# Kernel tuning notes

Hardware: AMD Instinct MI355X
Metric: run time of the kernel (lower is better)

Reference implementation:

```python
import jax, jax.numpy as jnp
import numpy as np
from jax import lax


def _qconv_w(r, i, j, k):
    # Hamilton-product block kernel: components are (out/4, in/4, kh, kw) -> (out, in, kh, kw)
    row_r = jnp.concatenate([r, -i, -j, -k], axis=1)
    row_i = jnp.concatenate([i, r, -k, j], axis=1)
    row_j = jnp.concatenate([j, k, r, -i], axis=1)
    row_k = jnp.concatenate([k, -j, i, r], axis=1)
    return jnp.concatenate([row_r, row_i, row_j, row_k], axis=0)


def _conv3x3(x, W, b):
    y = lax.conv_general_dilated(x, W, window_strides=(1, 1), padding=((1, 1), (1, 1)),
                                 dimension_numbers=('NCHW', 'OIHW', 'NCHW'))
    return y + b[None, :, None, None]


def _qbn(x, gamma, beta, eps=1e-5):
    # Quaternion BN: global per-component mean, shared scalar quaternion variance
    r, i, j, k = jnp.split(x, 4, axis=1)
    dr, di, dj, dk = r - r.mean(), i - i.mean(), j - j.mean(), k - k.mean()
    var = (dr * dr + di * di + dj * dj + dk * dk).mean()
    inv = 1.0 / jnp.sqrt(var + eps)
    br, bi, bj, bk = jnp.split(beta, 4, axis=1)
    return jnp.concatenate([gamma * dr * inv + br, gamma * di * inv + bi,
                            gamma * dj * inv + bj, gamma * dk * inv + bk], axis=1)


def _pool2(x):
    b, c, h, w = x.shape
    return x.reshape(b, c, h // 2, 2, w // 2, 2).mean(axis=(3, 5))


def _qlin_w(r, i, j, k):
    # components (in/4, out/4) -> (in, out)
    col_r = jnp.concatenate([r, -i, -j, -k], axis=0)
    col_i = jnp.concatenate([i, r, -k, j], axis=0)
    col_j = jnp.concatenate([j, k, r, -i], axis=0)
    col_k = jnp.concatenate([k, -j, i, r], axis=0)
    return jnp.concatenate([col_r, col_i, col_j, col_k], axis=1)


def _forward(x, w_eca, l1_r, l1_i, l1_j, l1_k, l1_b, bn1_gamma, bn1_beta,
             l2_r, l2_i, l2_j, l2_k, l2_b, bn2_gamma, bn2_beta,
             l3_r, l3_i, l3_j, l3_k, l3_b, bn3_gamma, bn3_beta,
             fc_r, fc_i, fc_j, fc_k, fc_b):
    # ---- pre_press: eca_layer(k_size=1) top-3 channel selection + zero quaternion channel
    pooled = x.mean(axis=(2, 3))                      # [B, C] global avg pool
    att = jax.nn.softmax(w_eca[0] * pooled, axis=1)   # 1x1 conv1d == scalar scale, softmax over channels
    _, idx = lax.top_k(att, 3)                        # sorted descending, matches torch.topk
    top3 = jnp.take_along_axis(x, idx[:, :, None, None], axis=1)  # [B, 3, H, W]
    q = jnp.concatenate([jnp.zeros_like(top3[:, :1]), top3], axis=1)  # [B, 4, H, W]
    # ---- QConvEtAl: only layer1..3 are used in forward
    h = _conv3x3(q, _qconv_w(l1_r, l1_i, l1_j, l1_k), l1_b)
    h = _pool2(jax.nn.relu(_qbn(h, bn1_gamma, bn1_beta)))
    h = _conv3x3(h, _qconv_w(l2_r, l2_i, l2_j, l2_k), l2_b)
    h = _pool2(jax.nn.relu(_qbn(h, bn2_gamma, bn2_beta)))
    h = _conv3x3(h, _qconv_w(l3_r, l3_i, l3_j, l3_k), l3_b)
    h = _pool2(jax.nn.relu(_qbn(h, bn3_gamma, bn3_beta)))
    h = h.reshape(h.shape[0], -1)                     # [B, 128*(P/8)^2]
    return h @ _qlin_w(fc_r, fc_i, fc_j, fc_k) + fc_b


def setup_inputs() -> dict:
    key = jax.random.key(0)
    ks = jax.random.split(key, 20)
    rn = lambda k, s, sc=0.1: (jax.random.normal(k, s) * sc).astype(jnp.float32)
    inp = {
        'x': jax.random.normal(ks[0], (256, 200, 32, 32), dtype=jnp.float32),
        'w_eca': rn(ks[1], (1,), 1.0),
        'l1_r': rn(ks[2], (4, 1, 3, 3)), 'l1_i': rn(ks[3], (4, 1, 3, 3)),
        'l1_j': rn(ks[4], (4, 1, 3, 3)), 'l1_k': rn(ks[5], (4, 1, 3, 3)),
        'l1_b': jnp.zeros((16,), jnp.float32),
        'bn1_gamma': jnp.ones((1, 4, 1, 1), jnp.float32), 'bn1_beta': jnp.zeros((1, 16, 1, 1), jnp.float32),
        'l2_r': rn(ks[6], (16, 4, 3, 3)), 'l2_i': rn(ks[7], (16, 4, 3, 3)),
        'l2_j': rn(ks[8], (16, 4, 3, 3)), 'l2_k': rn(ks[9], (16, 4, 3, 3)),
        'l2_b': jnp.zeros((64,), jnp.float32),
        'bn2_gamma': jnp.ones((1, 16, 1, 1), jnp.float32), 'bn2_beta': jnp.zeros((1, 64, 1, 1), jnp.float32),
        'l3_r': rn(ks[10], (32, 16, 3, 3)), 'l3_i': rn(ks[11], (32, 16, 3, 3)),
        'l3_j': rn(ks[12], (32, 16, 3, 3)), 'l3_k': rn(ks[13], (32, 16, 3, 3)),
        'l3_b': jnp.zeros((128,), jnp.float32),
        'bn3_gamma': jnp.ones((1, 32, 1, 1), jnp.float32), 'bn3_beta': jnp.zeros((1, 128, 1, 1), jnp.float32),
        'fc_r': rn(ks[14], (512, 4)), 'fc_i': rn(ks[15], (512, 4)),
        'fc_j': rn(ks[16], (512, 4)), 'fc_k': rn(ks[17], (512, 4)),
        'fc_b': jnp.zeros((16,), jnp.float32),
    }
    return inp


def reference(x, w_eca, l1_r, l1_i, l1_j, l1_k, l1_b, bn1_gamma, bn1_beta,
              l2_r, l2_i, l2_j, l2_k, l2_b, bn2_gamma, bn2_beta,
              l3_r, l3_i, l3_j, l3_k, l3_b, bn3_gamma, bn3_beta,
              fc_r, fc_i, fc_j, fc_k, fc_b):
    return _forward(x, w_eca, l1_r, l1_i, l1_j, l1_k, l1_b, bn1_gamma, bn1_beta,
                    l2_r, l2_i, l2_j, l2_k, l2_b, bn2_gamma, bn2_beta,
                    l3_r, l3_i, l3_j, l3_k, l3_b, bn3_gamma, bn3_beta,
                    fc_r, fc_i, fc_j, fc_k, fc_b)
```

## Files before the change

### kernel.cpp

```cpp
#include <hip/hip_runtime.h>
#include <math.h>

#define WS_STATS 0
#define WS_W1    32
#define WS_W2    640
#define WS_W3    9856
#define WS_WFC   83584
#define WS_POOL  116352
#define WS_IDX   167552
#define WS_OUT1  168448
#define WS_P1    4362752
#define WS_OUT3  5411328
#define WS_P3    7508480

__device__ const int   d_TC[4][4] = {{0,1,2,3},{1,0,3,2},{2,3,0,1},{3,2,1,0}};
__device__ const float d_TS[4][4] = {{1.f,-1.f,-1.f,-1.f},{1.f,1.f,-1.f,1.f},
                                     {1.f,1.f,1.f,-1.f},{1.f,-1.f,1.f,1.f}};

__global__ __launch_bounds__(256) void prep_kernel(
    const float* l1r, const float* l1i, const float* l1j, const float* l1k,
    const float* l2r, const float* l2i, const float* l2j, const float* l2k,
    const float* l3r, const float* l3i, const float* l3j, const float* l3k,
    const float* fcr, const float* fci, const float* fcj, const float* fck,
    float* ws)
{
    int tid  = blockIdx.x * 256 + threadIdx.x;
    int nthr = gridDim.x * 256;
    if (tid < 24) ws[WS_STATS + tid] = 0.f;

    {
        const float* cp[4] = {l1r, l1i, l1j, l1k};
        for (int e = tid; e < 576; e += nthr) {
            int s = e / 144, rem = e % 144, k = rem / 16, oc = rem % 16;
            int p = oc >> 2, o = oc & 3;
            ws[WS_W1 + e] = d_TS[p][s] * cp[d_TC[p][s]][o * 9 + k];
        }
    }
    {
        const float* cp[4] = {l2r, l2i, l2j, l2k};
        for (int e = tid; e < 9216; e += nthr) {
            int oc = e & 63, k = (e >> 6) % 9, ic = e / 576;
            int p = oc >> 4, o = oc & 15, s = ic >> 2, ii = ic & 3;
            ws[WS_W2 + e] = d_TS[p][s] * cp[d_TC[p][s]][(o * 4 + ii) * 9 + k];
        }
    }
    {
        const float* cp[4] = {l3r, l3i, l3j, l3k};
        for (int e = tid; e < 73728; e += nthr) {
            int oc = e & 127, k = (e >> 7) % 9, ic = e / 1152;
            int p = oc >> 5, o = oc & 31, s = ic >> 4, ii = ic & 15;
            ws[WS_W3 + e] = d_TS[p][s] * cp[d_TC[p][s]][(o * 16 + ii) * 9 + k];
        }
    }
    {
        const float* cp[4] = {fcr, fci, fcj, fck};
        for (int e = tid; e < 32768; e += nthr) {
            int R = e >> 4, C = e & 15;
            int p = R >> 9, rr = R & 511, q = C >> 2, cc = C & 3;
            ws[WS_WFC + e] = d_TS[q][p] * cp[d_TC[q][p]][rr * 4 + cc];
        }
    }
}

__global__ __launch_bounds__(256) void mean_kernel(const float* __restrict__ x,
                                                   float* __restrict__ pooled)
{
    int bc = blockIdx.x;
    int t  = threadIdx.x;
    const float4* src = reinterpret_cast<const float4*>(x + (size_t)bc * 1024);
    float4 v = src[t];
    float s = v.x + v.y + v.z + v.w;
    #pragma unroll
    for (int off = 32; off; off >>= 1) s += __shfl_xor(s, off, 64);
    __shared__ float red[4];
    if ((t & 63) == 0) red[t >> 6] = s;
    __syncthreads();
    if (t == 0) pooled[bc] = (red[0] + red[1] + red[2] + red[3]) * (1.0f / 1024.0f);
}

__global__ __launch_bounds__(64) void topk_kernel(const float* __restrict__ pooled,
                                                  const float* __restrict__ w_eca,
                                                  int* __restrict__ idx3)
{
    int b = blockIdx.x, lane = threadIdx.x;
    float w = w_eca[0];
    float v[4]; int c[4];
    #pragma unroll
    for (int i = 0; i < 4; i++) {
        int ch = lane + 64 * i;
        c[i] = ch;
        v[i] = (ch < 200) ? w * pooled[b * 200 + ch] : -INFINITY;
    }
    for (int k = 0; k < 3; k++) {
        float bv = -INFINITY; int bi = 0x3fffffff;
        #pragma unroll
        for (int i = 0; i < 4; i++)
            if (v[i] > bv || (v[i] == bv && c[i] < bi)) { bv = v[i]; bi = c[i]; }
        for (int off = 32; off; off >>= 1) {
            float ov = __shfl_xor(bv, off, 64);
            int   oi = __shfl_xor(bi, off, 64);
            if (ov > bv || (ov == bv && oi < bi)) { bv = ov; bi = oi; }
        }
        if (lane == 0) idx3[b * 3 + k] = bi;
        #pragma unroll
        for (int i = 0; i < 4; i++) if (c[i] == bi) v[i] = -INFINITY;
    }
}

__global__ __launch_bounds__(256) void conv1_kernel(const float* __restrict__ x,
                                                    const int* __restrict__ idx3,
                                                    const float* __restrict__ W1,
                                                    const float* __restrict__ b1,
                                                    float* __restrict__ out1,
                                                    float* __restrict__ stats)
{
    __shared__ float smem[3][6][36];
    __shared__ float rs[8];
    int b = blockIdx.x >> 3, rg = blockIdx.x & 7;
    int t = threadIdx.x;
    if (t < 8) rs[t] = 0.f;
    for (int i = t; i < 648; i += 256) {
        int s = i / 216, rem = i % 216, r = rem / 36, c = rem % 36;
        int gr = rg * 4 - 1 + r, gc = c - 1;
        float v = 0.f;
        if (gr >= 0 && gr < 32 && gc >= 0 && gc < 32)
            v = x[((size_t)b * 200 + idx3[b * 3 + s]) * 1024 + gr * 32 + gc];
        smem[s][r][c] = v;
    }
    __syncthreads();

    int oc = t & 15, rp = (t >> 4) & 3, ch = t >> 6;
    float bb = b1[oc];
    float acc[8];
    #pragma unroll
    for (int px = 0; px < 8; px++) acc[px] = bb;

    #pragma unroll
    for (int s = 0; s < 3; s++) {
        float w[9];
        #pragma unroll
        for (int k = 0; k < 9; k++) w[k] = W1[((s + 1) * 9 + k) * 16 + oc];
        float rowv[3][12];
        #pragma unroll
        for (int dy = 0; dy < 3; dy++) {
            const float* rb = &smem[s][rp + dy][ch * 8];
            float4 a = *reinterpret_cast<const float4*>(rb);
            float4 bq = *reinterpret_cast<const float4*>(rb + 4);
            float4 cq = *reinterpret_cast<const float4*>(rb + 8);
            rowv[dy][0]=a.x;  rowv[dy][1]=a.y;  rowv[dy][2]=a.z;  rowv[dy][3]=a.w;
            rowv[dy][4]=bq.x; rowv[dy][5]=bq.y; rowv[dy][6]=bq.z; rowv[dy][7]=bq.w;
            rowv[dy][8]=cq.x; rowv[dy][9]=cq.y; rowv[dy][10]=cq.z; rowv[dy][11]=cq.w;
        }
        #pragma unroll
        for (int dy = 0; dy < 3; dy++)
            #pragma unroll
            for (int px = 0; px < 8; px++) {
                float a = acc[px];
                a = fmaf(w[dy*3+0], rowv[dy][px],   a);
                a = fmaf(w[dy*3+1], rowv[dy][px+1], a);
                a = fmaf(w[dy*3+2], rowv[dy][px+2], a);
                acc[px] = a;
            }
    }
    int row = rg * 4 + rp;
    float* outb = out1 + ((size_t)b * 16 + oc) * 1024 + row * 32 + ch * 8;
    *reinterpret_cast<float4*>(outb)     = make_float4(acc[0], acc[1], acc[2], acc[3]);
    *reinterpret_cast<float4*>(outb + 4) = make_float4(acc[4], acc[5], acc[6], acc[7]);
    float sv = 0.f, qv = 0.f;
    #pragma unroll
    for (int px = 0; px < 8; px++) { sv += acc[px]; qv += acc[px] * acc[px]; }
    int g = oc >> 2;
    atomicAdd(&rs[g], sv); atomicAdd(&rs[4 + g], qv);
    __syncthreads();
    if (t < 8) atomicAdd(&stats[t], rs[t]);
}

template<int C, int H, int Cq>
__global__ __launch_bounds__(256) void bnpool_kernel(const float* __restrict__ in,
                                                     float* __restrict__ out,
                                                     const float* __restrict__ stats,
                                                     const float* __restrict__ gamma,
                                                     const float* __restrict__ beta,
                                                     float invN)
{
    constexpr int Ho = H / 2;
    int o = blockIdx.x * 256 + threadIdx.x;
    float mean[4]; float var = 0.f;
    #pragma unroll
    for (int g = 0; g < 4; g++) {
        float S = stats[g], Q = stats[4 + g];
        mean[g] = S * invN;
        var += Q - S * S * invN;
    }
    var *= invN;
    float inv = 1.0f / sqrtf(var + 1e-5f);

    int xq = o % Ho;
    int yq = (o / Ho) % Ho;
    int c  = (o / (Ho * Ho)) % C;
    int b  = o / (Ho * Ho * C);
    const float* base = in + ((size_t)((b * C + c) * H + 2 * yq)) * H + 2 * xq;
    float2 v01 = *reinterpret_cast<const float2*>(base);
    float2 v23 = *reinterpret_cast<const float2*>(base + H);
    int g = c / Cq, wv = c % Cq;
    float scale = gamma[wv] * inv;
    float sh = beta[c] - mean[g] * scale;
    float r0 = fmaxf(fmaf(v01.x, scale, sh), 0.f);
    float r1 = fmaxf(fmaf(v01.y, scale, sh), 0.f);
    float r2 = fmaxf(fmaf(v23.x, scale, sh), 0.f);
    float r3 = fmaxf(fmaf(v23.y, scale, sh), 0.f);
    out[o] = 0.25f * (r0 + r1 + r2 + r3);
}

__global__ __launch_bounds__(256) void conv2_kernel(const float* __restrict__ p1,
                                                    const float* __restrict__ W2,
                                                    const float* __restrict__ b2,
                                                    float* __restrict__ out2,
                                                    float* __restrict__ stats)
{
    __shared__ float smem[16][4][20];
    __shared__ float rs[8];
    int b = blockIdx.x >> 3, rq = blockIdx.x & 7;
    int t = threadIdx.x;
    if (t < 8) rs[t] = 0.f;
    for (int i = t; i < 1280; i += 256) {
        int ic = i / 80, rem = i % 80, r = rem / 20, c = rem % 20;
        int gr = rq * 2 - 1 + r, gc = c - 1;
        float v = 0.f;
        if (gr >= 0 && gr < 16 && gc >= 0 && gc < 16)
            v = p1[((size_t)b * 16 + ic) * 256 + gr * 16 + gc];
        smem[ic][r][c] = v;
    }
    __syncthreads();

    int oc = t & 63, rp = (t >> 6) & 1, ch = t >> 7;
    float bb = b2[oc];
    float acc[8];
    #pragma unroll
    for (int px = 0; px < 8; px++) acc[px] = bb;

    const float* Wp = W2 + oc;
    for (int ic = 0; ic < 16; ic++) {
        float w[9];
        #pragma unroll
        for (int k = 0; k < 9; k++) w[k] = Wp[ic * 576 + k * 64];
        float rowv[3][12];
        #pragma unroll
        for (int dy = 0; dy < 3; dy++) {
            const float* rb = &smem[ic][rp + dy][ch * 8];
            float4 a = *reinterpret_cast<const float4*>(rb);
            float4 bq = *reinterpret_cast<const float4*>(rb + 4);
            float4 cq = *reinterpret_cast<const float4*>(rb + 8);
            rowv[dy][0]=a.x;  rowv[dy][1]=a.y;  rowv[dy][2]=a.z;  rowv[dy][3]=a.w;
            rowv[dy][4]=bq.x; rowv[dy][5]=bq.y; rowv[dy][6]=bq.z; rowv[dy][7]=bq.w;
            rowv[dy][8]=cq.x; rowv[dy][9]=cq.y; rowv[dy][10]=cq.z; rowv[dy][11]=cq.w;
        }
        #pragma unroll
        for (int dy = 0; dy < 3; dy++)
            #pragma unroll
            for (int px = 0; px < 8; px++) {
                float a = acc[px];
                a = fmaf(w[dy*3+0], rowv[dy][px],   a);
                a = fmaf(w[dy*3+1], rowv[dy][px+1], a);
                a = fmaf(w[dy*3+2], rowv[dy][px+2], a);
                acc[px] = a;
            }
    }
    int row = rq * 2 + rp;
    float* outb = out2 + ((size_t)b * 64 + oc) * 256 + row * 16 + ch * 8;
    *reinterpret_cast<float4*>(outb)     = make_float4(acc[0], acc[1], acc[2], acc[3]);
    *reinterpret_cast<float4*>(outb + 4) = make_float4(acc[4], acc[5], acc[6], acc[7]);
    float sv = 0.f, qv = 0.f;
    #pragma unroll
    for (int px = 0; px < 8; px++) { sv += acc[px]; qv += acc[px] * acc[px]; }
    int g = oc >> 4;
    atomicAdd(&rs[g], sv); atomicAdd(&rs[4 + g], qv);
    __syncthreads();
    if (t < 8) atomicAdd(&stats[t], rs[t]);
}

__global__ __launch_bounds__(256) void conv3_kernel(const float* __restrict__ p2,
                                                    const float* __restrict__ W3,
                                                    const float* __restrict__ b3,
                                                    float* __restrict__ out3,
                                                    float* __restrict__ stats)
{
    __shared__ float smem[64][4][12];
    __shared__ float rs[8];
    int b = blockIdx.x >> 2, rh = blockIdx.x & 3;
    int t = threadIdx.x;
    if (t < 8) rs[t] = 0.f;
    for (int i = t; i < 3072; i += 256) {
        int ic = i / 48, rem = i % 48, r = rem / 12, c = rem % 12;
        int gr = rh * 2 - 1 + r, gc = c - 1;
        float v = 0.f;
        if (gr >= 0 && gr < 8 && gc >= 0 && gc < 8)
            v = p2[((size_t)b * 64 + ic) * 64 + gr * 8 + gc];
        smem[ic][r][c] = v;
    }
    __syncthreads();

    int oc = t & 127, rp = t >> 7;
    float bb = b3[oc];
    float acc[8];
    #pragma unroll
    for (int px = 0; px < 8; px++) acc[px] = bb;

    const float* Wp = W3 + oc;
    float w[9], wn[9];
    #pragma unroll
    for (int k = 0; k < 9; k++) w[k] = Wp[k * 128];
    for (int ic = 0; ic < 64; ic++) {
        if (ic < 63) {
            #pragma unroll
            for (int k = 0; k < 9; k++) wn[k] = Wp[(ic + 1) * 1152 + k * 128];
        }
        float rowv[3][12];
        #pragma unroll
        for (int dy = 0; dy < 3; dy++) {
            const float* rb = &smem[ic][rp + dy][0];
            float4 a = *reinterpret_cast<const float4*>(rb);
            float4 bq = *reinterpret_cast<const float4*>(rb + 4);
            float4 cq = *reinterpret_cast<const float4*>(rb + 8);
            rowv[dy][0]=a.x;  rowv[dy][1]=a.y;  rowv[dy][2]=a.z;  rowv[dy][3]=a.w;
            rowv[dy][4]=bq.x; rowv[dy][5]=bq.y; rowv[dy][6]=bq.z; rowv[dy][7]=bq.w;
            rowv[dy][8]=cq.x; rowv[dy][9]=cq.y; rowv[dy][10]=cq.z; rowv[dy][11]=cq.w;
        }
        #pragma unroll
        for (int dy = 0; dy < 3; dy++)
            #pragma unroll
            for (int px = 0; px < 8; px++) {
                float a = acc[px];
                a = fmaf(w[dy*3+0], rowv[dy][px],   a);
                a = fmaf(w[dy*3+1], rowv[dy][px+1], a);
                a = fmaf(w[dy*3+2], rowv[dy][px+2], a);
                acc[px] = a;
            }
        if (ic < 63) {
            #pragma unroll
            for (int k = 0; k < 9; k++) w[k] = wn[k];
        }
    }
    int row = rh * 2 + rp;
    float* outb = out3 + ((size_t)b * 128 + oc) * 64 + row * 8;
    *reinterpret_cast<float4*>(outb)     = make_float4(acc[0], acc[1], acc[2], acc[3]);
    *reinterpret_cast<float4*>(outb + 4) = make_float4(acc[4], acc[5], acc[6], acc[7]);
    float sv = 0.f, qv = 0.f;
    #pragma unroll
    for (int px = 0; px < 8; px++) { sv += acc[px]; qv += acc[px] * acc[px]; }
    int g = oc >> 5;
    atomicAdd(&rs[g], sv); atomicAdd(&rs[4 + g], qv);
    __syncthreads();
    if (t < 8) atomicAdd(&stats[t], rs[t]);
}

__global__ __launch_bounds__(256) void fc_kernel(const float* __restrict__ p3,
                                                 const float* __restrict__ WFC,
                                                 const float* __restrict__ fcb,
                                                 float* __restrict__ out)
{
    int b = blockIdx.x, t = threadIdx.x;
    int col = t & 15, fr = t >> 4;
    const float* pb = p3 + (size_t)b * 2048;
    float s = 0.f;
    for (int i = 0; i < 128; i++) {
        int f = i * 16 + fr;
        s = fmaf(pb[f], WFC[f * 16 + col], s);
    }
    __shared__ float red[256];
    red[t] = s;
    __syncthreads();
    for (int st = 128; st >= 16; st >>= 1) {
        if (t < st) red[t] += red[t + st];
        __syncthreads();
    }
    if (t < 16) out[b * 16 + t] = red[t] + fcb[t];
}

extern "C" void kernel_launch(void* const* d_in, const int* in_sizes, int n_in,
                              void* d_out, int out_size, void* d_ws, size_t ws_size,
                              hipStream_t stream)
{
    (void)in_sizes; (void)n_in; (void)out_size; (void)ws_size;
    const float* x     = (const float*)d_in[0];
    const float* w_eca = (const float*)d_in[1];
    const float* l1r = (const float*)d_in[2],  *l1i = (const float*)d_in[3];
    const float* l1j = (const float*)d_in[4],  *l1k = (const float*)d_in[5];
    const float* l1b = (const float*)d_in[6];
    const float* bn1g = (const float*)d_in[7], *bn1b = (const float*)d_in[8];
    const float* l2r = (const float*)d_in[9],  *l2i = (const float*)d_in[10];
    const float* l2j = (const float*)d_in[11], *l2k = (const float*)d_in[12];
    const float* l2b = (const float*)d_in[13];
    const float* bn2g = (const float*)d_in[14], *bn2b = (const float*)d_in[15];
    const float* l3r = (const float*)d_in[16], *l3i = (const float*)d_in[17];
    const float* l3j = (const float*)d_in[18], *l3k = (const float*)d_in[19];
    const float* l3b = (const float*)d_in[20];
    const float* bn3g = (const float*)d_in[21], *bn3b = (const float*)d_in[22];
    const float* fcr = (const float*)d_in[23], *fci = (const float*)d_in[24];
    const float* fcj = (const float*)d_in[25], *fck = (const float*)d_in[26];
    const float* fcb = (const float*)d_in[27];

    float* ws   = (float*)d_ws;
    float* outp = (float*)d_out;

    prep_kernel<<<512, 256, 0, stream>>>(l1r, l1i, l1j, l1k, l2r, l2i, l2j, l2k,
                                         l3r, l3i, l3j, l3k, fcr, fci, fcj, fck, ws);
    mean_kernel<<<51200, 256, 0, stream>>>(x, ws + WS_POOL);
    topk_kernel<<<256, 64, 0, stream>>>(ws + WS_POOL, w_eca, (int*)(ws + WS_IDX));
    conv1_kernel<<<2048, 256, 0, stream>>>(x, (const int*)(ws + WS_IDX), ws + WS_W1,
                                           l1b, ws + WS_OUT1, ws + WS_STATS);
    bnpool_kernel<16, 32, 4><<<4096, 256, 0, stream>>>(ws + WS_OUT1, ws + WS_P1,
        ws + WS_STATS, bn1g, bn1b, 1.0f / 1048576.0f);
    conv2_kernel<<<2048, 256, 0, stream>>>(ws + WS_P1, ws + WS_W2, l2b,
                                           ws + WS_OUT1, ws + WS_STATS + 8);
    bnpool_kernel<64, 16, 16><<<4096, 256, 0, stream>>>(ws + WS_OUT1, ws + WS_P1,
        ws + WS_STATS + 8, bn2g, bn2b, 1.0f / 1048576.0f);
    conv3_kernel<<<1024, 256, 0, stream>>>(ws + WS_P1, ws + WS_W3, l3b,
                                           ws + WS_OUT3, ws + WS_STATS + 16);
    bnpool_kernel<128, 8, 32><<<2048, 256, 0, stream>>>(ws + WS_OUT3, ws + WS_P3,
        ws + WS_STATS + 16, bn3g, bn3b, 1.0f / 524288.0f);
    fc_kernel<<<256, 256, 0, stream>>>(ws + WS_P3, ws + WS_WFC, fcb, outp);
}
```

Baseline: 190.9 us.

## Fuse BN+pool into consumer convs, merge prep/mean and topk into conv1

Cuts the launch chain from ten kernels to five. The BN-ReLU-avgpool stages are folded into the shared-memory loads of conv2, conv3 and fc, and the weight prep is merged with the channel-mean pass. Top-k selection now runs inside each conv1 block. This removes the pooled intermediate buffers and their extra global round trips. In exchange, the top-k is recomputed redundantly in every block (8 per batch), and conv2 gets register double-buffering of its weights.

```diff
diff --git a/kernel.cpp b/kernel.cpp
--- a/kernel.cpp
+++ b/kernel.cpp
@@ -7,25 +7,38 @@
 #define WS_W3    9856
 #define WS_WFC   83584
 #define WS_POOL  116352
-#define WS_IDX   167552
-#define WS_OUT1  168448
-#define WS_P1    4362752
-#define WS_OUT3  5411328
-#define WS_P3    7508480
+#define WS_OUT1  167552
+#define WS_OUT2  4361856
+#define WS_OUT3  8556160
 
 __device__ const int   d_TC[4][4] = {{0,1,2,3},{1,0,3,2},{2,3,0,1},{3,2,1,0}};
 __device__ const float d_TS[4][4] = {{1.f,-1.f,-1.f,-1.f},{1.f,1.f,-1.f,1.f},
                                      {1.f,1.f,1.f,-1.f},{1.f,-1.f,1.f,1.f}};
 
-__global__ __launch_bounds__(256) void prep_kernel(
+__global__ __launch_bounds__(256) void prepmean_kernel(
+    const float* __restrict__ x, float* __restrict__ pooled,
     const float* l1r, const float* l1i, const float* l1j, const float* l1k,
     const float* l2r, const float* l2i, const float* l2j, const float* l2k,
     const float* l3r, const float* l3i, const float* l3j, const float* l3k,
     const float* fcr, const float* fci, const float* fcj, const float* fck,
     float* ws)
 {
-    int tid  = blockIdx.x * 256 + threadIdx.x;
-    int nthr = gridDim.x * 256;
+    __shared__ float red[4];
+    int bid = blockIdx.x;
+    int t = threadIdx.x;
+    if (bid < 51200) {
+        const float4* src = reinterpret_cast<const float4*>(x + (size_t)bid * 1024);
+        float4 v = src[t];
+        float s = v.x + v.y + v.z + v.w;
+        #pragma unroll
+        for (int off = 32; off; off >>= 1) s += __shfl_xor(s, off, 64);
+        if ((t & 63) == 0) red[t >> 6] = s;
+        __syncthreads();
+        if (t == 0) pooled[bid] = (red[0] + red[1] + red[2] + red[3]) * (1.0f / 1024.0f);
+        return;
+    }
+    int tid = (bid - 51200) * 256 + t;
+    const int nthr = 512 * 256;
     if (tid < 24) ws[WS_STATS + tid] = 0.f;
 
     {
@@ -62,53 +75,9 @@
     }
 }
 
-__global__ __launch_bounds__(256) void mean_kernel(const float* __restrict__ x,
-                                                   float* __restrict__ pooled)
-{
-    int bc = blockIdx.x;
-    int t  = threadIdx.x;
-    const float4* src = reinterpret_cast<const float4*>(x + (size_t)bc * 1024);
-    float4 v = src[t];
-    float s = v.x + v.y + v.z + v.w;
-    #pragma unroll
-    for (int off = 32; off; off >>= 1) s += __shfl_xor(s, off, 64);
-    __shared__ float red[4];
-    if ((t & 63) == 0) red[t >> 6] = s;
-    __syncthreads();
-    if (t == 0) pooled[bc] = (red[0] + red[1] + red[2] + red[3]) * (1.0f / 1024.0f);
-}
-
-__global__ __launch_bounds__(64) void topk_kernel(const float* __restrict__ pooled,
-                                                  const float* __restrict__ w_eca,
-                                                  int* __restrict__ idx3)
-{
-    int b = blockIdx.x, lane = threadIdx.x;
-    float w = w_eca[0];
-    float v[4]; int c[4];
-    #pragma unroll
-    for (int i = 0; i < 4; i++) {
-        int ch = lane + 64 * i;
-        c[i] = ch;
-        v[i] = (ch < 200) ? w * pooled[b * 200 + ch] : -INFINITY;
-    }
-    for (int k = 0; k < 3; k++) {
-        float bv = -INFINITY; int bi = 0x3fffffff;
-        #pragma unroll
-        for (int i = 0; i < 4; i++)
-            if (v[i] > bv || (v[i] == bv && c[i] < bi)) { bv = v[i]; bi = c[i]; }
-        for (int off = 32; off; off >>= 1) {
-            float ov = __shfl_xor(bv, off, 64);
-            int   oi = __shfl_xor(bi, off, 64);
-            if (ov > bv || (ov == bv && oi < bi)) { bv = ov; bi = oi; }
-        }
-        if (lane == 0) idx3[b * 3 + k] = bi;
-        #pragma unroll
-        for (int i = 0; i < 4; i++) if (c[i] == bi) v[i] = -INFINITY;
-    }
-}
-
 __global__ __launch_bounds__(256) void conv1_kernel(const float* __restrict__ x,
-                                                    const int* __restrict__ idx3,
+                                                    const float* __restrict__ pooled,
+                                                    const float* __restrict__ w_eca,
                                                     const float* __restrict__ W1,
                                                     const float* __restrict__ b1,
                                                     float* __restrict__ out1,
@@ -116,16 +85,42 @@
 {
     __shared__ float smem[3][6][36];
     __shared__ float rs[8];
+    __shared__ int idx_s[3];
     int b = blockIdx.x >> 3, rg = blockIdx.x & 7;
     int t = threadIdx.x;
     if (t < 8) rs[t] = 0.f;
+    if (t < 64) {
+        float w = w_eca[0];
+        float v[4]; int c[4];
+        #pragma unroll
+        for (int i = 0; i < 4; i++) {
+            int ch = t + 64 * i;
+            c[i] = ch;
+            v[i] = (ch < 200) ? w * pooled[b * 200 + ch] : -INFINITY;
+        }
+        for (int k = 0; k < 3; k++) {
+            float bv = -INFINITY; int bi = 0x3fffffff;
+            #pragma unroll
+            for (int i = 0; i < 4; i++)
+                if (v[i] > bv || (v[i] == bv && c[i] < bi)) { bv = v[i]; bi = c[i]; }
+            for (int off = 32; off; off >>= 1) {
+                float ov = __shfl_xor(bv, off, 64);
+                int   oi = __shfl_xor(bi, off, 64);
+                if (ov > bv || (ov == bv && oi < bi)) { bv = ov; bi = oi; }
+            }
+            if (t == 0) idx_s[k] = bi;
+            #pragma unroll
+            for (int i = 0; i < 4; i++) if (c[i] == bi) v[i] = -INFINITY;
+        }
+    }
+    __syncthreads();
     for (int i = t; i < 648; i += 256) {
-        int s = i / 216, rem = i % 216, r = rem / 36, c = rem % 36;
-        int gr = rg * 4 - 1 + r, gc = c - 1;
+        int s = i / 216, rem = i % 216, r = rem / 36, cc = rem % 36;
+        int gr = rg * 4 - 1 + r, gc = cc - 1;
         float v = 0.f;
         if (gr >= 0 && gr < 32 && gc >= 0 && gc < 32)
-            v = x[((size_t)b * 200 + idx3[b * 3 + s]) * 1024 + gr * 32 + gc];
-        smem[s][r][c] = v;
+            v = x[((size_t)b * 200 + idx_s[s]) * 1024 + gr * 32 + gc];
+        smem[s][r][cc] = v;
     }
     __syncthreads();
 
@@ -175,61 +170,48 @@
     if (t < 8) atomicAdd(&stats[t], rs[t]);
 }
 
-template<int C, int H, int Cq>
-__global__ __launch_bounds__(256) void bnpool_kernel(const float* __restrict__ in,
-                                                     float* __restrict__ out,
-                                                     const float* __restrict__ stats,
-                                                     const float* __restrict__ gamma,
-                                                     const float* __restrict__ beta,
-                                                     float invN)
-{
-    constexpr int Ho = H / 2;
-    int o = blockIdx.x * 256 + threadIdx.x;
-    float mean[4]; float var = 0.f;
-    #pragma unroll
-    for (int g = 0; g < 4; g++) {
-        float S = stats[g], Q = stats[4 + g];
-        mean[g] = S * invN;
-        var += Q - S * S * invN;
-    }
-    var *= invN;
-    float inv = 1.0f / sqrtf(var + 1e-5f);
-
-    int xq = o % Ho;
-    int yq = (o / Ho) % Ho;
-    int c  = (o / (Ho * Ho)) % C;
-    int b  = o / (Ho * Ho * C);
-    const float* base = in + ((size_t)((b * C + c) * H + 2 * yq)) * H + 2 * xq;
-    float2 v01 = *reinterpret_cast<const float2*>(base);
-    float2 v23 = *reinterpret_cast<const float2*>(base + H);
-    int g = c / Cq, wv = c % Cq;
-    float scale = gamma[wv] * inv;
-    float sh = beta[c] - mean[g] * scale;
-    float r0 = fmaxf(fmaf(v01.x, scale, sh), 0.f);
-    float r1 = fmaxf(fmaf(v01.y, scale, sh), 0.f);
-    float r2 = fmaxf(fmaf(v23.x, scale, sh), 0.f);
-    float r3 = fmaxf(fmaf(v23.y, scale, sh), 0.f);
-    out[o] = 0.25f * (r0 + r1 + r2 + r3);
-}
-
-__global__ __launch_bounds__(256) void conv2_kernel(const float* __restrict__ p1,
+__global__ __launch_bounds__(256) void conv2_kernel(const float* __restrict__ out1,
                                                     const float* __restrict__ W2,
                                                     const float* __restrict__ b2,
+                                                    const float* __restrict__ bn1g,
+                                                    const float* __restrict__ bn1b,
                                                     float* __restrict__ out2,
                                                     float* __restrict__ stats)
 {
     __shared__ float smem[16][4][20];
     __shared__ float rs[8];
+    __shared__ float sc[16], sh[16];
     int b = blockIdx.x >> 3, rq = blockIdx.x & 7;
     int t = threadIdx.x;
     if (t < 8) rs[t] = 0.f;
+    if (t < 16) {
+        const float invN = 1.0f / 1048576.0f;
+        float var = 0.f;
+        #pragma unroll
+        for (int g = 0; g < 4; g++) {
+            float S = stats[g], Q = stats[4 + g];
+            var += Q - S * S * invN;
+        }
+        var *= invN;
+        float inv = 1.0f / sqrtf(var + 1e-5f);
+        float scale = bn1g[t & 3] * inv;
+        sc[t] = scale;
+        sh[t] = bn1b[t] - stats[t >> 2] * invN * scale;
+    }
+    __syncthreads();
     for (int i = t; i < 1280; i += 256) {
-        int ic = i / 80, rem = i % 80, r = rem / 20, c = rem % 20;
-        int gr = rq * 2 - 1 + r, gc = c - 1;
+        int ic = i / 80, rem = i % 80, r = rem / 20, cc = rem % 20;
+        int gr = rq * 2 - 1 + r, gc = cc - 1;
         float v = 0.f;
-        if (gr >= 0 && gr < 16 && gc >= 0 && gc < 16)
-            v = p1[((size_t)b * 16 + ic) * 256 + gr * 16 + gc];
-        smem[ic][r][c] = v;
+        if (gr >= 0 && gr < 16 && gc >= 0 && gc < 16) {
+            const float* base = out1 + ((size_t)(b * 16 + ic) * 32 + 2 * gr) * 32 + 2 * gc;
+            float2 a = *reinterpret_cast<const float2*>(base);
+            float2 d = *reinterpret_cast<const float2*>(base + 32);
+            float s0 = sc[ic], s1 = sh[ic];
+            v = 0.25f * (fmaxf(fmaf(a.x, s0, s1), 0.f) + fmaxf(fmaf(a.y, s0, s1), 0.f)
+                       + fmaxf(fmaf(d.x, s0, s1), 0.f) + fmaxf(fmaf(d.y, s0, s1), 0.f));
+        }
+        smem[ic][r][cc] = v;
     }
     __syncthreads();
 
@@ -240,10 +222,14 @@
     for (int px = 0; px < 8; px++) acc[px] = bb;
 
     const float* Wp = W2 + oc;
+    float w[9], wn[9];
+    #pragma unroll
+    for (int k = 0; k < 9; k++) w[k] = Wp[k * 64];
     for (int ic = 0; ic < 16; ic++) {
-        float w[9];
-        #pragma unroll
-        for (int k = 0; k < 9; k++) w[k] = Wp[ic * 576 + k * 64];
+        if (ic < 15) {
+            #pragma unroll
+            for (int k = 0; k < 9; k++) wn[k] = Wp[(ic + 1) * 576 + k * 64];
+        }
         float rowv[3][12];
         #pragma unroll
         for (int dy = 0; dy < 3; dy++) {
@@ -265,6 +251,10 @@
                 a = fmaf(w[dy*3+2], rowv[dy][px+2], a);
                 acc[px] = a;
             }
+        if (ic < 15) {
+            #pragma unroll
+            for (int k = 0; k < 9; k++) w[k] = wn[k];
+        }
     }
     int row = rq * 2 + rp;
     float* outb = out2 + ((size_t)b * 64 + oc) * 256 + row * 16 + ch * 8;
@@ -276,27 +266,51 @@
     int g = oc >> 4;
     atomicAdd(&rs[g], sv); atomicAdd(&rs[4 + g], qv);
     __syncthreads();
-    if (t < 8) atomicAdd(&stats[t], rs[t]);
-}
-
-__global__ __launch_bounds__(256) void conv3_kernel(const float* __restrict__ p2,
+    if (t < 8) atomicAdd(&stats[8 + t], rs[t]);
+}
+
+__global__ __launch_bounds__(256) void conv3_kernel(const float* __restrict__ out2,
                                                     const float* __restrict__ W3,
                                                     const float* __restrict__ b3,
+                                                    const float* __restrict__ bn2g,
+                                                    const float* __restrict__ bn2b,
                                                     float* __restrict__ out3,
                                                     float* __restrict__ stats)
 {
     __shared__ float smem[64][4][12];
     __shared__ float rs[8];
+    __shared__ float sc[64], sh[64];
     int b = blockIdx.x >> 2, rh = blockIdx.x & 3;
     int t = threadIdx.x;
     if (t < 8) rs[t] = 0.f;
+    if (t < 64) {
+        const float invN = 1.0f / 1048576.0f;
+        float var = 0.f;
+        #pragma unroll
+        for (int g = 0; g < 4; g++) {
+            float S = stats[8 + g], Q = stats[12 + g];
+            var += Q - S * S * invN;
+        }
+        var *= invN;
+        float inv = 1.0f / sqrtf(var + 1e-5f);
+        float scale = bn2g[t & 15] * inv;
+        sc[t] = scale;
+        sh[t] = bn2b[t] - stats[8 + (t >> 4)] * invN * scale;
+    }
+    __syncthreads();
     for (int i = t; i < 3072; i += 256) {
-        int ic = i / 48, rem = i % 48, r = rem / 12, c = rem % 12;
-        int gr = rh * 2 - 1 + r, gc = c - 1;
+        int ic = i / 48, rem = i % 48, r = rem / 12, cc = rem % 12;
+        int gr = rh * 2 - 1 + r, gc = cc - 1;
         float v = 0.f;
-        if (gr >= 0 && gr < 8 && gc >= 0 && gc < 8)
-            v = p2[((size_t)b * 64 + ic) * 64 + gr * 8 + gc];
-        smem[ic][r][c] = v;
+        if (gr >= 0 && gr < 8 && gc >= 0 && gc < 8) {
+            const float* base = out2 + ((size_t)(b * 64 + ic) * 16 + 2 * gr) * 16 + 2 * gc;
+            float2 a = *reinterpret_cast<const float2*>(base);
+            float2 d = *reinterpret_cast<const float2*>(base + 16);
+            float s0 = sc[ic], s1 = sh[ic];
+            v = 0.25f * (fmaxf(fmaf(a.x, s0, s1), 0.f) + fmaxf(fmaf(a.y, s0, s1), 0.f)
+                       + fmaxf(fmaf(d.x, s0, s1), 0.f) + fmaxf(fmaf(d.y, s0, s1), 0.f));
+        }
+        smem[ic][r][cc] = v;
     }
     __syncthreads();
 
@@ -351,23 +365,52 @@
     int g = oc >> 5;
     atomicAdd(&rs[g], sv); atomicAdd(&rs[4 + g], qv);
     __syncthreads();
-    if (t < 8) atomicAdd(&stats[t], rs[t]);
-}
-
-__global__ __launch_bounds__(256) void fc_kernel(const float* __restrict__ p3,
+    if (t < 8) atomicAdd(&stats[16 + t], rs[t]);
+}
+
+__global__ __launch_bounds__(256) void fc_kernel(const float* __restrict__ out3,
                                                  const float* __restrict__ WFC,
                                                  const float* __restrict__ fcb,
+                                                 const float* __restrict__ bn3g,
+                                                 const float* __restrict__ bn3b,
+                                                 const float* __restrict__ stats,
                                                  float* __restrict__ out)
 {
+    __shared__ float p3s[2048];
+    __shared__ float sc[128], sh[128];
+    __shared__ float red[256];
     int b = blockIdx.x, t = threadIdx.x;
+    if (t < 128) {
+        const float invN = 1.0f / 524288.0f;
+        float var = 0.f;
+        #pragma unroll
+        for (int g = 0; g < 4; g++) {
+            float S = stats[16 + g], Q = stats[20 + g];
+            var += Q - S * S * invN;
+        }
+        var *= invN;
+        float inv = 1.0f / sqrtf(var + 1e-5f);
+        float scale = bn3g[t & 31] * inv;
+        sc[t] = scale;
+        sh[t] = bn3b[t] - stats[16 + (t >> 5)] * invN * scale;
+    }
+    __syncthreads();
+    for (int i = t; i < 2048; i += 256) {
+        int c = i >> 4, rem = i & 15, pr = rem >> 2, pc = rem & 3;
+        const float* base = out3 + ((size_t)(b * 128 + c) * 8 + 2 * pr) * 8 + 2 * pc;
+        float2 a = *reinterpret_cast<const float2*>(base);
+        float2 d = *reinterpret_cast<const float2*>(base + 8);
+        float s0 = sc[c], s1 = sh[c];
+        p3s[i] = 0.25f * (fmaxf(fmaf(a.x, s0, s1), 0.f) + fmaxf(fmaf(a.y, s0, s1), 0.f)
+                        + fmaxf(fmaf(d.x, s0, s1), 0.f) + fmaxf(fmaf(d.y, s0, s1), 0.f));
+    }
+    __syncthreads();
     int col = t & 15, fr = t >> 4;
-    const float* pb = p3 + (size_t)b * 2048;
     float s = 0.f;
     for (int i = 0; i < 128; i++) {
         int f = i * 16 + fr;
-        s = fmaf(pb[f], WFC[f * 16 + col], s);
-    }
-    __shared__ float red[256];
+        s = fmaf(p3s[f], WFC[f * 16 + col], s);
+    }
     red[t] = s;
     __syncthreads();
     for (int st = 128; st >= 16; st >>= 1) {
@@ -403,21 +446,15 @@
     float* ws   = (float*)d_ws;
     float* outp = (float*)d_out;
 
-    prep_kernel<<<512, 256, 0, stream>>>(l1r, l1i, l1j, l1k, l2r, l2i, l2j, l2k,
-                                         l3r, l3i, l3j, l3k, fcr, fci, fcj, fck, ws);
-    mean_kernel<<<51200, 256, 0, stream>>>(x, ws + WS_POOL);
-    topk_kernel<<<256, 64, 0, stream>>>(ws + WS_POOL, w_eca, (int*)(ws + WS_IDX));
-    conv1_kernel<<<2048, 256, 0, stream>>>(x, (const int*)(ws + WS_IDX), ws + WS_W1,
+    prepmean_kernel<<<51712, 256, 0, stream>>>(x, ws + WS_POOL,
+        l1r, l1i, l1j, l1k, l2r, l2i, l2j, l2k, l3r, l3i, l3j, l3k,
+        fcr, fci, fcj, fck, ws);
+    conv1_kernel<<<2048, 256, 0, stream>>>(x, ws + WS_POOL, w_eca, ws + WS_W1,
                                            l1b, ws + WS_OUT1, ws + WS_STATS);
-    bnpool_kernel<16, 32, 4><<<4096, 256, 0, stream>>>(ws + WS_OUT1, ws + WS_P1,
-        ws + WS_STATS, bn1g, bn1b, 1.0f / 1048576.0f);
-    conv2_kernel<<<2048, 256, 0, stream>>>(ws + WS_P1, ws + WS_W2, l2b,
-                                           ws + WS_OUT1, ws + WS_STATS + 8);
-    bnpool_kernel<64, 16, 16><<<4096, 256, 0, stream>>>(ws + WS_OUT1, ws + WS_P1,
-        ws + WS_STATS + 8, bn2g, bn2b, 1.0f / 1048576.0f);
-    conv3_kernel<<<1024, 256, 0, stream>>>(ws + WS_P1, ws + WS_W3, l3b,
-                                           ws + WS_OUT3, ws + WS_STATS + 16);
-    bnpool_kernel<128, 8, 32><<<2048, 256, 0, stream>>>(ws + WS_OUT3, ws + WS_P3,
-        ws + WS_STATS + 16, bn3g, bn3b, 1.0f / 524288.0f);
-    fc_kernel<<<256, 256, 0, stream>>>(ws + WS_P3, ws + WS_WFC, fcb, outp);
-}
+    conv2_kernel<<<2048, 256, 0, stream>>>(ws + WS_OUT1, ws + WS_W2, l2b, bn1g, bn1b,
+                                           ws + WS_OUT2, ws + WS_STATS);
+    conv3_kernel<<<1024, 256, 0, stream>>>(ws + WS_OUT2, ws + WS_W3, l3b, bn2g, bn2b,
+                                           ws + WS_OUT3, ws + WS_STATS);
+    fc_kernel<<<256, 256, 0, stream>>>(ws + WS_OUT3, ws + WS_WFC, fcb, bn3g, bn3b,
+                                       ws + WS_STATS, outp);
+}
```

Result: faster. 185.1 us (-3.0%).
